# Kernel tuning notes

Hardware: AMD Instinct MI355X
Metric: run time of the kernel (lower is better)

## Reference

```python
import math
import jax, jax.numpy as jnp
import numpy as np
from jax import lax

# ---- fixed (non-learned) kernels, built exactly as in Canny.__init__ ----
def _sobel_2d(k=5):
    r = np.linspace(-(k // 2), k // 2, k).astype(np.float32)
    x, y = np.meshgrid(r, r, indexing='ij')
    den = x ** 2 + y ** 2
    den[:, k // 2] = 1.0
    return (x / den / 6.0).astype(np.float32)

_S = _sobel_2d(5)
W_SY = jnp.asarray(_S.reshape(1, 1, 5, 5))            # sobel_y weight
W_SX = jnp.asarray(_S.T.reshape(1, 1, 5, 5))          # sobel_x weight (transposed)

_pos = [(0, 1), (2, 1), (1, 0), (1, 2), (0, 0), (2, 2), (0, 2), (2, 0)]
_ksel = np.zeros((8, 1, 3, 3), dtype=np.float32)
for _i, (_a, _b) in enumerate(_pos):
    _ksel[_i, 0, _a, _b] = 1.0
W_SEL = jnp.asarray(_ksel)
SEL_IDS = jnp.asarray(np.array([[0, 1], [4, 5], [2, 3], [6, 7],
                                [0, 1], [4, 5], [2, 3], [6, 7]], dtype=np.int32))
W_HYST = jnp.ones((1, 1, 3, 3), dtype=jnp.float32)

_DN = ('NCHW', 'OIHW', 'NCHW')

def _conv_reflect(x, w, pad):
    x = jnp.pad(x, ((0, 0), (0, 0), (pad, pad), (pad, pad)), mode='reflect')
    return lax.conv_general_dilated(x, w, (1, 1), 'VALID', dimension_numbers=_DN)

def _conv_zero(x, w, pad):
    return lax.conv_general_dilated(x, w, (1, 1), ((pad, pad), (pad, pad)),
                                    dimension_numbers=_DN)

THRESH_LO = 0.1
THRESH_HI = 0.1

def setup_inputs() -> dict:
    key = jax.random.key(0)
    images = jax.random.uniform(key, (16, 3, 512, 512), dtype=jnp.float32)
    return {'images': images}

def reference(images):
    # shift from [-1,1] to [0,1] if needed
    images = jnp.where(images.min() < -0.001, (images + 1.0) * 0.5, images)
    # channel L2 norm -> [B,1,H,W], normalize by global max
    mag = jnp.linalg.norm(images, axis=1, keepdims=True)
    mag = mag / mag.max()
    sobel_x = _conv_reflect(mag, W_SX, 2)
    sobel_y = _conv_reflect(mag, W_SY, 2)
    grad_mag = jnp.sqrt(sobel_x ** 2 + sobel_y ** 2)             # [B,1,H,W]
    phase = jnp.arctan2(sobel_x, sobel_y + 1e-5)
    phase = jnp.mod(jnp.round(phase / (math.pi / 4)) + 4.0, 8.0).astype(jnp.int32)
    selections = _conv_zero(grad_mag, W_SEL, 1)                  # [B,8,H,W]
    neb_ids = SEL_IDS[phase[:, 0]]                               # [B,H,W,2]
    nebs = jnp.take_along_axis(selections, jnp.transpose(neb_ids, (0, 3, 1, 2)), axis=1)
    # phase-dependent non-maximum suppression
    mask = (grad_mag <= nebs[:, 0:1]) | (grad_mag < nebs[:, 1:2])
    grad_mag = jnp.where(mask, 0.0, grad_mag)
    # low threshold
    grad_mag = jnp.where(grad_mag < THRESH_LO, 0.0, grad_mag)
    # hysteresis
    weak_mask = (grad_mag < THRESH_HI) & (grad_mag > THRESH_LO)
    high_mask = grad_mag > THRESH_HI
    high_nebs = _conv_reflect(high_mask.astype(jnp.float32), W_HYST, 1)
    weak_keep = weak_mask & (high_nebs > 0)
    kill = (~weak_keep) & (~high_mask)
    grad_mag = jnp.where(kill, 0.0, grad_mag)
    # String_Finder: binarize edges at 0.1
    b_edges = jnp.where(grad_mag > 0.1, 1.0, 0.0)
    sobel = jnp.concatenate([sobel_y, sobel_x], axis=1)          # [B,2,H,W]
    return b_edges, sobel
```

## Files before the change

### kernel.cpp

```cpp
#include <hip/hip_runtime.h>
#include <math.h>

#define HH 512
#define WW 512
#define HW (HH*WW)

__device__ __forceinline__ int refl(int i) {
  if (i < 0) return -i;
  if (i >= HH) return 2*HH - 2 - i;
  return i;
}

__device__ __forceinline__ float sumsq3(float r, float g, float b) {
  return __fadd_rn(__fadd_rn(__fmul_rn(r,r), __fmul_rn(g,g)), __fmul_rn(b,b));
}

__global__ __launch_bounds__(256) void k1_sumsq(const float* __restrict__ img,
                                                float* __restrict__ ss,
                                                float* __restrict__ partials) {
  int gid = blockIdx.x * 256 + threadIdx.x;
  int n  = gid >> 16;
  int p4 = gid & 65535;
  const float* base = img + (size_t)n * 3 * HW;
  float4 r = ((const float4*)(base        ))[p4];
  float4 g = ((const float4*)(base +   HW ))[p4];
  float4 b = ((const float4*)(base + 2*HW ))[p4];
  float4 s;
  s.x = sumsq3(r.x, g.x, b.x);
  s.y = sumsq3(r.y, g.y, b.y);
  s.z = sumsq3(r.z, g.z, b.z);
  s.w = sumsq3(r.w, g.w, b.w);
  ((float4*)ss)[gid] = s;

  float m = fmaxf(fmaxf(s.x, s.y), fmaxf(s.z, s.w));
  #pragma unroll
  for (int off = 32; off > 0; off >>= 1)
    m = fmaxf(m, __shfl_down(m, off));
  __shared__ float sm[4];
  int lane = threadIdx.x & 63, wv = threadIdx.x >> 6;
  if (lane == 0) sm[wv] = m;
  __syncthreads();
  if (threadIdx.x == 0)
    partials[blockIdx.x] = fmaxf(fmaxf(sm[0], sm[1]), fmaxf(sm[2], sm[3]));
}

__global__ __launch_bounds__(256) void k1b_reduce(const float* __restrict__ partials,
                                                  float* __restrict__ ssmax) {
  float m = 0.0f;
  #pragma unroll
  for (int i = 0; i < 16; ++i)
    m = fmaxf(m, partials[threadIdx.x + 256 * i]);
  #pragma unroll
  for (int off = 32; off > 0; off >>= 1)
    m = fmaxf(m, __shfl_down(m, off));
  __shared__ float sm[4];
  int lane = threadIdx.x & 63, wv = threadIdx.x >> 6;
  if (lane == 0) sm[wv] = m;
  __syncthreads();
  if (threadIdx.x == 0)
    ssmax[0] = fmaxf(fmaxf(sm[0], sm[1]), fmaxf(sm[2], sm[3]));
}

__global__ __launch_bounds__(256) void k3_sobel(const float* __restrict__ ss,
                                                const float* __restrict__ ssmax,
                                                float* __restrict__ sobel_out,
                                                float* __restrict__ gm,
                                                unsigned char* __restrict__ pairb) {
  __shared__ float magS[20 * 68];
  int tx = threadIdx.x;
  int ty = threadIdx.y;
  int x0 = blockIdx.x * 64;
  int y0 = blockIdx.y * 16;
  int n  = blockIdx.z;
  const float* sp = ss + (size_t)n * HW;
  float mm = sqrtf(ssmax[0]);

  int tid = ty * 64 + tx;
  for (int i = tid; i < 20 * 68; i += 256) {
    int r = i / 68, c = i - r * 68;
    int gy = refl(y0 - 2 + r);
    int gx = refl(x0 - 2 + c);
    magS[i] = __fdiv_rn(sqrtf(sp[gy * WW + gx]), mm);
  }
  __syncthreads();

  const double wA0 = (double)(-2.0f/8.0f/6.0f);
  const double wA1 = (double)(-2.0f/5.0f/6.0f);
  const double wA2 = (double)(-2.0f/1.0f/6.0f);
  const double wB0 = (double)(-1.0f/5.0f/6.0f);
  const double wB1 = (double)(-1.0f/2.0f/6.0f);
  const double wB2 = (double)(-1.0f/1.0f/6.0f);

  double S[8], T[8], C[8], D0[8], D1[8];
  #pragma unroll
  for (int j = 0; j < 8; ++j) {
    const float* rowp = &magS[(4 * ty + j) * 68 + tx];
    double v0 = (double)rowp[0], v1 = (double)rowp[1], v2 = (double)rowp[2],
           v3 = (double)rowp[3], v4 = (double)rowp[4];
    S[j]  = v0 + v4;  T[j]  = v1 + v3;  C[j] = v2;
    D0[j] = v0 - v4;  D1[j] = v1 - v3;
  }

  int x = x0 + tx;
  #pragma unroll
  for (int dy = 0; dy < 4; ++dy) {
    int r = 4 * ty + dy;
    int y = y0 + r;
    int j = dy;
    double asy = wA0*(S[j]-S[j+4]) + wA1*(T[j]-T[j+4]) + wA2*(C[j]-C[j+4])
               + wB0*(S[j+1]-S[j+3]) + wB1*(T[j+1]-T[j+3]) + wB2*(C[j+1]-C[j+3]);
    double asx = wA0*(D0[j]+D0[j+4]) + wA1*(D0[j+1]+D0[j+3]) + wA2*D0[j+2]
               + wB0*(D1[j]+D1[j+4]) + wB1*(D1[j+1]+D1[j+3]) + wB2*D1[j+2];
    float fsy = (float)asy, fsx = (float)asx;
    int p = y * WW + x;
    sobel_out[(size_t)n * 2 * HW + p]      = fsy;
    sobel_out[(size_t)n * 2 * HW + HW + p] = fsx;
    float g = sqrtf(__fadd_rn(__fmul_rn(fsx, fsx), __fmul_rn(fsy, fsy)));
    gm[(size_t)n * HW + p] = g;
    float ph = atan2f(fsx, __fadd_rn(fsy, 1e-5f));
    float pf = __fdiv_rn(ph, 0.78539816339744830962f);
    float rr = rintf(pf);
    int ip = ((int)rr + 4) & 7;
    pairb[(size_t)n * HW + p] = (unsigned char)(ip & 3);
  }
}

__global__ __launch_bounds__(256) void k4_nms(const float* __restrict__ gm,
                                              const unsigned char* __restrict__ pairb,
                                              float* __restrict__ edges) {
  int x = blockIdx.x * 64 + threadIdx.x;
  int y = blockIdx.y * 4  + threadIdx.y;
  int n = blockIdx.z;
  const float* gp = gm + (size_t)n * HW;
  int p = y * WW + x;
  float g = gp[p];
  int pr = pairb[(size_t)n * HW + p];
  const int dy0[4] = {-1, -1,  0, -1};
  const int dx0[4] = { 0, -1, -1,  1};
  const int dy1[4] = { 1,  1,  0,  1};
  const int dx1[4] = { 0,  1,  1, -1};
  int y0 = y + dy0[pr], x0 = x + dx0[pr];
  int y1 = y + dy1[pr], x1 = x + dx1[pr];
  float n0 = (y0 >= 0 && y0 < HH && x0 >= 0 && x0 < WW) ? gp[y0 * WW + x0] : 0.0f;
  float n1 = (y1 >= 0 && y1 < HH && x1 >= 0 && x1 < WW) ? gp[y1 * WW + x1] : 0.0f;
  bool mask = (g <= n0) || (g < n1);
  edges[(size_t)n * HW + p] = (!mask && (g > 0.1f)) ? 1.0f : 0.0f;
}

extern "C" void kernel_launch(void* const* d_in, const int* in_sizes, int n_in,
                              void* d_out, int out_size, void* d_ws, size_t ws_size,
                              hipStream_t stream) {
  const float* img = (const float*)d_in[0];
  float* out = (float*)d_out;
  char* ws = (char*)d_ws;

  float* ssmax    = (float*)ws;
  float* partials = (float*)(ws + 256);
  float* ssbuf    = (float*)(ws + 256 + 16384);
  float* gm       = (float*)(ws + 256 + 16384 + 16777216);
  unsigned char* pairb = (unsigned char*)(ws + 256 + 16384 + 2*16777216);

  float* edges = out;
  float* sobel = out + 4194304;

  k1_sumsq  <<<dim3(4096), dim3(256), 0, stream>>>(img, ssbuf, partials);
  k1b_reduce<<<dim3(1),    dim3(256), 0, stream>>>(partials, ssmax);
  k3_sobel<<<dim3(8, 32, 16), dim3(64, 4), 0, stream>>>(ssbuf, ssmax, sobel, gm, pairb);
  k4_nms  <<<dim3(8, 128, 16), dim3(64, 4), 0, stream>>>(gm, pairb, edges);
}
```

Before: 130.7 us.

## Fuse Sobel and NMS kernels using overlapping halo tiles in shared memory

Merges the Sobel/gradient kernel with the non-maximum-suppression kernel. Each block now computes a 64x16 gradient tile that includes a one-pixel halo and writes a 62x14 interior of outputs. Gradient magnitudes stay in shared memory and the phase pair is packed into registers, so the global gm and pairb buffers and one launch are removed. In exchange, the halo pixels are computed redundantly and the grid has more blocks (9x37 instead of 8x32), and the stores are less aligned because the tile width is no longer 64.

```diff
diff --git a/kernel.cpp b/kernel.cpp
--- a/kernel.cpp
+++ b/kernel.cpp
@@ -4,6 +4,9 @@
 #define HH 512
 #define WW 512
 #define HW (HH*WW)
+
+#define OTW 62
+#define OTH 14
 
 __device__ __forceinline__ int refl(int i) {
   if (i < 0) return -i;
@@ -61,16 +64,16 @@
     ssmax[0] = fmaxf(fmaxf(sm[0], sm[1]), fmaxf(sm[2], sm[3]));
 }
 
-__global__ __launch_bounds__(256) void k3_sobel(const float* __restrict__ ss,
-                                                const float* __restrict__ ssmax,
-                                                float* __restrict__ sobel_out,
-                                                float* __restrict__ gm,
-                                                unsigned char* __restrict__ pairb) {
+__global__ __launch_bounds__(256) void k34_sobel_nms(const float* __restrict__ ss,
+                                                     const float* __restrict__ ssmax,
+                                                     float* __restrict__ sobel_out,
+                                                     float* __restrict__ edges) {
   __shared__ float magS[20 * 68];
+  __shared__ float gmS[16 * 64];
   int tx = threadIdx.x;
   int ty = threadIdx.y;
-  int x0 = blockIdx.x * 64;
-  int y0 = blockIdx.y * 16;
+  int ox0 = blockIdx.x * OTW;
+  int oy0 = blockIdx.y * OTH;
   int n  = blockIdx.z;
   const float* sp = ss + (size_t)n * HW;
   float mm = sqrtf(ssmax[0]);
@@ -78,8 +81,8 @@
   int tid = ty * 64 + tx;
   for (int i = tid; i < 20 * 68; i += 256) {
     int r = i / 68, c = i - r * 68;
-    int gy = refl(y0 - 2 + r);
-    int gx = refl(x0 - 2 + c);
+    int gy = refl(oy0 - 3 + r);
+    int gx = refl(ox0 - 3 + c);
     magS[i] = __fdiv_rn(sqrtf(sp[gy * WW + gx]), mm);
   }
   __syncthreads();
@@ -101,50 +104,57 @@
     D0[j] = v0 - v4;  D1[j] = v1 - v3;
   }
 
-  int x = x0 + tx;
+  int x = ox0 - 1 + tx;
+  bool xin = (tx >= 1) && (tx <= OTW) && (x < WW);
+  int prpack = 0;
   #pragma unroll
   for (int dy = 0; dy < 4; ++dy) {
     int r = 4 * ty + dy;
-    int y = y0 + r;
+    int y = oy0 - 1 + r;
     int j = dy;
     double asy = wA0*(S[j]-S[j+4]) + wA1*(T[j]-T[j+4]) + wA2*(C[j]-C[j+4])
                + wB0*(S[j+1]-S[j+3]) + wB1*(T[j+1]-T[j+3]) + wB2*(C[j+1]-C[j+3]);
     double asx = wA0*(D0[j]+D0[j+4]) + wA1*(D0[j+1]+D0[j+3]) + wA2*D0[j+2]
                + wB0*(D1[j]+D1[j+4]) + wB1*(D1[j+1]+D1[j+3]) + wB2*D1[j+2];
     float fsy = (float)asy, fsx = (float)asx;
-    int p = y * WW + x;
-    sobel_out[(size_t)n * 2 * HW + p]      = fsy;
-    sobel_out[(size_t)n * 2 * HW + HW + p] = fsx;
     float g = sqrtf(__fadd_rn(__fmul_rn(fsx, fsx), __fmul_rn(fsy, fsy)));
-    gm[(size_t)n * HW + p] = g;
+    gmS[r * 64 + tx] = g;
     float ph = atan2f(fsx, __fadd_rn(fsy, 1e-5f));
     float pf = __fdiv_rn(ph, 0.78539816339744830962f);
     float rr = rintf(pf);
     int ip = ((int)rr + 4) & 7;
-    pairb[(size_t)n * HW + p] = (unsigned char)(ip & 3);
+    prpack |= (ip & 3) << (2 * dy);
+    if (xin && r >= 1 && r <= OTH && y < HH) {
+      int p = y * WW + x;
+      sobel_out[(size_t)n * 2 * HW + p]      = fsy;
+      sobel_out[(size_t)n * 2 * HW + HW + p] = fsx;
+    }
   }
-}
+  __syncthreads();
 
-__global__ __launch_bounds__(256) void k4_nms(const float* __restrict__ gm,
-                                              const unsigned char* __restrict__ pairb,
-                                              float* __restrict__ edges) {
-  int x = blockIdx.x * 64 + threadIdx.x;
-  int y = blockIdx.y * 4  + threadIdx.y;
-  int n = blockIdx.z;
-  const float* gp = gm + (size_t)n * HW;
-  int p = y * WW + x;
-  float g = gp[p];
-  int pr = pairb[(size_t)n * HW + p];
-  const int dy0[4] = {-1, -1,  0, -1};
-  const int dx0[4] = { 0, -1, -1,  1};
-  const int dy1[4] = { 1,  1,  0,  1};
-  const int dx1[4] = { 0,  1,  1, -1};
-  int y0 = y + dy0[pr], x0 = x + dx0[pr];
-  int y1 = y + dy1[pr], x1 = x + dx1[pr];
-  float n0 = (y0 >= 0 && y0 < HH && x0 >= 0 && x0 < WW) ? gp[y0 * WW + x0] : 0.0f;
-  float n1 = (y1 >= 0 && y1 < HH && x1 >= 0 && x1 < WW) ? gp[y1 * WW + x1] : 0.0f;
-  bool mask = (g <= n0) || (g < n1);
-  edges[(size_t)n * HW + p] = (!mask && (g > 0.1f)) ? 1.0f : 0.0f;
+  if (xin) {
+    const int dy0[4] = {-1, -1,  0, -1};
+    const int dx0[4] = { 0, -1, -1,  1};
+    const int dy1[4] = { 1,  1,  0,  1};
+    const int dx1[4] = { 0,  1,  1, -1};
+    #pragma unroll
+    for (int dy = 0; dy < 4; ++dy) {
+      int r = 4 * ty + dy;
+      if (r < 1 || r > OTH) continue;
+      int y = oy0 - 1 + r;
+      if (y >= HH) continue;
+      int pr = (prpack >> (2 * dy)) & 3;
+      float g = gmS[r * 64 + tx];
+      int yy0 = y + dy0[pr], xx0 = x + dx0[pr];
+      int yy1 = y + dy1[pr], xx1 = x + dx1[pr];
+      float n0 = (yy0 >= 0 && yy0 < HH && xx0 >= 0 && xx0 < WW)
+                   ? gmS[(r + dy0[pr]) * 64 + (tx + dx0[pr])] : 0.0f;
+      float n1 = (yy1 >= 0 && yy1 < HH && xx1 >= 0 && xx1 < WW)
+                   ? gmS[(r + dy1[pr]) * 64 + (tx + dx1[pr])] : 0.0f;
+      bool mask = (g <= n0) || (g < n1);
+      edges[(size_t)n * HW + y * WW + x] = (!mask && (g > 0.1f)) ? 1.0f : 0.0f;
+    }
+  }
 }
 
 extern "C" void kernel_launch(void* const* d_in, const int* in_sizes, int n_in,
@@ -157,14 +167,12 @@
   float* ssmax    = (float*)ws;
   float* partials = (float*)(ws + 256);
   float* ssbuf    = (float*)(ws + 256 + 16384);
-  float* gm       = (float*)(ws + 256 + 16384 + 16777216);
-  unsigned char* pairb = (unsigned char*)(ws + 256 + 16384 + 2*16777216);
 
   float* edges = out;
   float* sobel = out + 4194304;
 
   k1_sumsq  <<<dim3(4096), dim3(256), 0, stream>>>(img, ssbuf, partials);
   k1b_reduce<<<dim3(1),    dim3(256), 0, stream>>>(partials, ssmax);
-  k3_sobel<<<dim3(8, 32, 16), dim3(64, 4), 0, stream>>>(ssbuf, ssmax, sobel, gm, pairb);
-  k4_nms  <<<dim3(8, 128, 16), dim3(64, 4), 0, stream>>>(gm, pairb, edges);
+  k34_sobel_nms<<<dim3((WW + OTW - 1) / OTW, (HH + OTH - 1) / OTH, 16),
+                  dim3(64, 4), 0, stream>>>(ssbuf, ssmax, sobel, edges);
 }
```

Result: faster. 125.0 us (-4.4%).
